# Kernel optimization log

Hardware: AMD Instinct MI355X
Metric: run time of the kernel (lower is better)

The kernel has to match this reference:

```python
import jax, jax.numpy as jnp
from jax import lax
import numpy as np

# NOTE: the original module calls an opaque CUDA 'approximate dot-product' conv kernel.
# Its backward uses EXACT conv2d gradients for input/weight, so the reference forward
# math is the exact conv2d the kernel approximates. `approximate` is a learned scalar
# controlling the hardware approximation level; it does not change the exact-math output.

STRIDE = 1
PAD = (1, 1)  # (padH, padW)


def setup_inputs() -> dict:
    key = jax.random.key(0)
    k1, k2, k3 = jax.random.split(key, 3)
    B, Cin, H, W = 32, 128, 56, 56
    Cout, K = 256, 3
    x = jax.random.normal(k1, (B, Cin, H, W), dtype=jnp.float32)
    # weight init: uniform(-1, 1) per reset_parameters
    weight = jax.random.uniform(k2, (Cout, Cin, K, K), dtype=jnp.float32, minval=-1.0, maxval=1.0)
    fan_in = Cin * K * K
    bound = 1.0 / np.sqrt(fan_in)
    bias = jax.random.uniform(k3, (Cout,), dtype=jnp.float32, minval=-bound, maxval=bound)
    approximate = jnp.ones((1,), dtype=jnp.float32)
    return {"x": x, "weight": weight, "bias": bias, "approximate": approximate}


def reference(x, weight, bias, approximate):
    # Exact conv2d, NCHW input, OIHW kernel. `approximate` controls only the
    # hardware approximation level in the original CUDA kernel.
    out = lax.conv_general_dilated(
        x, weight,
        window_strides=(STRIDE, STRIDE),
        padding=((PAD[0], PAD[0]), (PAD[1], PAD[1])),
        dimension_numbers=("NCHW", "OIHW", "NCHW"),
    )
    return out + bias.reshape(1, -1, 1, 1)
```

## Files before the change

### kernel.cpp

```cpp
#include <hip/hip_runtime.h>


typedef __attribute__((ext_vector_type(8))) short short8;
typedef __attribute__((ext_vector_type(4))) float floatx4;

typedef __attribute__((address_space(1))) const void* gas_ptr;
typedef __attribute__((address_space(3))) void* las_ptr;

__device__ static inline void gl2lds16(const void* g, void* l) {
    __builtin_amdgcn_global_load_lds((gas_ptr)g, (las_ptr)l, 16, 0, 0);
}

__device__ static inline float bf2f(unsigned short u) {
    union { unsigned int i; float f; } x; x.i = ((unsigned int)u) << 16; return x.f;
}
__device__ static inline unsigned short f2bf(float f) {
    union { float f; unsigned int i; } x; x.f = f;
    unsigned int r = (x.i + 0x7FFFu + ((x.i >> 16) & 1u)) >> 16;
    return (unsigned short)r;
}

__device__ static inline bool wave_detect_bf16(const unsigned int* __restrict__ p) {
    const int lane = threadIdx.x & 63;
    int cnt = 0;
#pragma unroll
    for (int r = 0; r < 4; ++r) {
        unsigned int w = p[r * 64 + lane];
        unsigned short lo = (unsigned short)(w & 0xFFFFu);
        int e = (lo >> 7) & 0xFF;
        bool plaus = (lo == 0) || (e >= 96 && e <= 144);
        cnt += (int)__popcll(__ballot(plaus));
    }
    return cnt >= 205;
}

__global__ void wt_repack(const void* __restrict__ wsrc,
                          unsigned short* __restrict__ wt) {
    const bool isbf = wave_detect_bf16((const unsigned int*)wsrc);
    int idx = blockIdx.x * 256 + threadIdx.x;
    int ci  = idx & 127;
    int co  = (idx >> 7) & 255;
    int off = idx >> 15;
    size_t s = (size_t)(co * 128 + ci) * 9 + off;
    float v = isbf ? bf2f(((const unsigned short*)wsrc)[s])
                   : ((const float*)wsrc)[s];
    wt[idx] = f2bf(v);
}

__global__ __launch_bounds__(256) void x_repack(
    const void* __restrict__ xsrc, unsigned short* __restrict__ xp) {
    __shared__ unsigned short tile[56 * 130];
    const int bh  = blockIdx.x;
    const int b   = bh / 58, hp = bh - b * 58;
    const int tid = threadIdx.x;
    unsigned short* row = xp + (size_t)(b * 58 + hp) * 58 * 128;
    if (hp == 0 || hp == 57) {
        uint4 z; z.x = z.y = z.z = z.w = 0u;
        uint4* r = (uint4*)row;
        for (int t = tid; t < 928; t += 256) r[t] = z;
        return;
    }
    const bool isbf = wave_detect_bf16((const unsigned int*)xsrc);
    const int h = hp - 1;
    if (isbf) {
        const unsigned short* xs =
            (const unsigned short*)xsrc + (size_t)b * 128 * 3136 + h * 56;
#pragma unroll
        for (int it = 0; it < 7; ++it) {
            int idx = it * 256 + tid;
            int ci = idx / 14, w4 = idx - ci * 14;
            ushort4 v = *(const ushort4*)(xs + (size_t)ci * 3136 + w4 * 4);
            tile[(w4 * 4 + 0) * 130 + ci] = v.x;
            tile[(w4 * 4 + 1) * 130 + ci] = v.y;
            tile[(w4 * 4 + 2) * 130 + ci] = v.z;
            tile[(w4 * 4 + 3) * 130 + ci] = v.w;
        }
    } else {
        const float* xs = (const float*)xsrc + (size_t)b * 128 * 3136 + h * 56;
#pragma unroll
        for (int it = 0; it < 7; ++it) {
            int idx = it * 256 + tid;
            int ci = idx / 14, w4 = idx - ci * 14;
            float4 v = *(const float4*)(xs + (size_t)ci * 3136 + w4 * 4);
            tile[(w4 * 4 + 0) * 130 + ci] = f2bf(v.x);
            tile[(w4 * 4 + 1) * 130 + ci] = f2bf(v.y);
            tile[(w4 * 4 + 2) * 130 + ci] = f2bf(v.z);
            tile[(w4 * 4 + 3) * 130 + ci] = f2bf(v.w);
        }
    }
    __syncthreads();
#pragma unroll
    for (int it = 0; it < 4; ++it) {
        int k = it * 256 + tid;
        if (k >= 928) break;
        int wq = k >> 4, cc = k & 15;
        uint4 v;
        if (wq == 0 || wq == 57) { v.x = v.y = v.z = v.w = 0u; }
        else {
            const unsigned short* p = &tile[(wq - 1) * 130 + cc * 8];
            union { unsigned short s[8]; uint4 u; } pk;
#pragma unroll
            for (int j = 0; j < 8; ++j) pk.s[j] = p[j];
            v = pk.u;
        }
        *(uint4*)(row + wq * 128 + cc * 8) = v;
    }
}

__global__ __launch_bounds__(256, 2) void conv_mfma(
    const unsigned short* __restrict__ xp,
    const unsigned short* __restrict__ wt,
    const void* __restrict__ bias,
    void* __restrict__ out,
    const void* __restrict__ xorig)
{
    __shared__ __align__(16) char lds[73728];
    const int tid   = threadIdx.x;
    const int lane  = tid & 63;
    const int wv    = tid >> 6;
    const int bid   = blockIdx.x;
    const int ntile = (bid & 7) * 98 + (bid >> 3);

    const bool isbf = wave_detect_bf16((const unsigned int*)xorig);

    const int clg  = (lane & 3) ^ ((lane >> 3) & 3);
    const int rsub = lane >> 2;
    unsigned sbA[4], sbB[2];
    int dbA[4], dbB[2];
#pragma unroll
    for (int s = 0; s < 4; ++s) {
        const int c  = wv * 4 + s;
        const int co = c * 16 + rsub;
        sbA[s] = (unsigned)(co * 256 + clg * 16);
        dbA[s] = c * 1024;
    }
#pragma unroll
    for (int s = 0; s < 2; ++s) {
        const int c = wv * 2 + s;
        const int n = ntile * 128 + c * 16 + rsub;
        const int b = n / 3136, rem = n - b * 3136;
        const int hh = rem / 56, ww = rem - hh * 56;
        sbB[s] = (unsigned)(((b * 58 + hh) * 58 + ww) * 256 + clg * 16);
        dbB[s] = 16384 + c * 1024;
    }

    const int fr = lane & 15;
    const int ph = (lane >> 4) ^ ((fr >> 1) & 3);
    const int wm = wv >> 1;
    const int wn = wv & 1;
    const int aOff = (wm * 128 + fr) * 64 + ph * 16;
    const int bOff = 16384 + (wn * 64 + fr) * 64 + ph * 16;

    floatx4 acc[8][4] = {};

#pragma unroll
    for (int h = 0; h < 2; ++h) {
        char* lb = lds + h * 24576;
        const int q = h & 3;
        const int dA  = q * 64;
        const int dB  = q * 64;
#pragma unroll
        for (int s = 0; s < 4; ++s)
            gl2lds16((const char*)wt + sbA[s] + dA, lb + dbA[s]);
#pragma unroll
        for (int s = 0; s < 2; ++s)
            gl2lds16((const char*)xp + sbB[s] + dB, lb + dbB[s]);
    }
    __builtin_amdgcn_s_waitcnt(0x3F76);
    __builtin_amdgcn_s_barrier();

    int bf_ = 0, st_ = 2;
#pragma unroll 3
    for (int h = 0; h < 36; ++h) {
        const char* la = lds + bf_ * 24576;
        if (h < 34) {
            char* sd = lds + st_ * 24576;
            const int hn  = h + 2;
            const int off = hn >> 2, q = hn & 3;
            const int dA  = off * 65536 + q * 64;
            const int dh_ = off / 3, dw_ = off - dh_ * 3;
            const int dB  = (dh_ * 58 + dw_) * 256 + q * 64;
#pragma unroll
            for (int s = 0; s < 4; ++s)
                gl2lds16((const char*)wt + sbA[s] + dA, sd + dbA[s]);
#pragma unroll
            for (int s = 0; s < 2; ++s)
                gl2lds16((const char*)xp + sbB[s] + dB, sd + dbB[s]);
        }
        short8 af[8], bf[4];
#pragma unroll
        for (int i = 0; i < 8; ++i)
            af[i] = *(const short8*)(la + aOff + i * 1024);
#pragma unroll
        for (int j = 0; j < 4; ++j)
            bf[j] = *(const short8*)(la + bOff + j * 1024);
        __builtin_amdgcn_s_setprio(1);
#pragma unroll
        for (int i = 0; i < 8; ++i)
#pragma unroll
            for (int j = 0; j < 4; ++j)
                acc[i][j] = __builtin_amdgcn_mfma_f32_16x16x32_bf16(
                    af[i], bf[j], acc[i][j], 0, 0, 0);
        __builtin_amdgcn_s_setprio(0);
        if (h < 34) {
            __builtin_amdgcn_s_waitcnt(0x3F76);
            __builtin_amdgcn_s_barrier();
        } else if (h == 34) {
            __builtin_amdgcn_s_waitcnt(0x3F70);
            __builtin_amdgcn_s_barrier();
        }
        bf_ = (bf_ == 2) ? 0 : bf_ + 1;
        st_ = (st_ == 2) ? 0 : st_ + 1;
    }

    const int q4 = (lane >> 4) << 2;
    int nb[4], ns[4];
#pragma unroll
    for (int j = 0; j < 4; ++j) {
        const int n = ntile * 128 + wn * 64 + j * 16 + fr;
        nb[j] = n / 3136;
        ns[j] = n - nb[j] * 3136;
    }
#pragma unroll
    for (int i = 0; i < 8; ++i) {
        const int co = wm * 128 + i * 16 + q4;
        float bv[4];
        if (isbf) {
            const ushort4 bb = *(const ushort4*)((const unsigned short*)bias + co);
            bv[0] = bf2f(bb.x); bv[1] = bf2f(bb.y);
            bv[2] = bf2f(bb.z); bv[3] = bf2f(bb.w);
        } else {
            const float4 bb = *(const float4*)((const float*)bias + co);
            bv[0] = bb.x; bv[1] = bb.y; bv[2] = bb.z; bv[3] = bb.w;
        }
#pragma unroll
        for (int j = 0; j < 4; ++j) {
#pragma unroll
            for (int r = 0; r < 4; ++r) {
                const float v = acc[i][j][r] + bv[r];
                const size_t o = (size_t)nb[j] * 802816 +
                                 (size_t)(co + r) * 3136 + ns[j];
                if (isbf) ((unsigned short*)out)[o] = f2bf(v);
                else      ((float*)out)[o] = v;
            }
        }
    }
}

__global__ void conv_naive(const float* __restrict__ x,
                           const float* __restrict__ w,
                           const float* __restrict__ bias,
                           float* __restrict__ out) {
    long long i = (long long)blockIdx.x * 256 + threadIdx.x;
    if (i >= 25690112LL) return;
    int wo = (int)(i % 56); long long t = i / 56;
    int ho = (int)(t % 56); t /= 56;
    int co = (int)(t % 256); int b = (int)(t / 256);
    float acc = bias[co];
    for (int ci = 0; ci < 128; ++ci)
        for (int dh = 0; dh < 3; ++dh) {
            int hi = ho + dh - 1; if ((unsigned)hi >= 56u) continue;
            for (int dw = 0; dw < 3; ++dw) {
                int wi = wo + dw - 1; if ((unsigned)wi >= 56u) continue;
                acc += x[((size_t)(b * 128 + ci) * 56 + hi) * 56 + wi] *
                       w[((co * 128 + ci) * 3 + dh) * 3 + dw];
            }
        }
    out[i] = acc;
}

extern "C" void kernel_launch(void* const* d_in, const int* in_sizes, int n_in,
                              void* d_out, int out_size, void* d_ws, size_t ws_size,
                              hipStream_t stream) {
    const void* x    = d_in[0];
    const void* w    = d_in[1];
    const void* bias = d_in[2];

    const size_t xp_bytes = (size_t)32 * 58 * 58 * 128 * 2;
    const size_t wt_off   = xp_bytes;
    const size_t wt_bytes = (size_t)9 * 256 * 128 * 2;
    const size_t need     = wt_off + wt_bytes;

    if (ws_size >= need) {
        unsigned short* xp = (unsigned short*)d_ws;
        unsigned short* wt = (unsigned short*)((char*)d_ws + wt_off);
        x_repack<<<32 * 58, 256, 0, stream>>>(x, xp);
        wt_repack<<<1152, 256, 0, stream>>>(w, wt);
        conv_mfma<<<dim3(784, 1, 1), 256, 0, stream>>>(xp, wt, bias, d_out, x);
    } else {
        conv_naive<<<(25690112 + 255) / 256, 256, 0, stream>>>(
            (const float*)x, (const float*)w, (const float*)bias, (float*)d_out);
    }
}
```

Measured before the change: 210.6 us.

## Load weight fragments directly to registers, pre-swizzled, and shrink LDS to input double buffer

The weight repack now writes the weights in MFMA fragment order, so each lane can load its A operands straight from global memory (L2-resident) into registers, double-buffered across iterations. Only the input tile stays in LDS, now a two-stage buffer of 16 KB instead of a three-stage 72 KB buffer. This removes weight traffic through LDS and LDS reads for A, and lowers the shared-memory footprint so more blocks can be resident. In exchange, every wave issues its own global weight loads each iteration, adding latency on the critical path, and the loop keeps 16 extra fragment registers live.

```diff
diff --git a/kernel.cpp b/kernel.cpp
--- a/kernel.cpp
+++ b/kernel.cpp
@@ -37,14 +37,23 @@
 __global__ void wt_repack(const void* __restrict__ wsrc,
                           unsigned short* __restrict__ wt) {
     const bool isbf = wave_detect_bf16((const unsigned int*)wsrc);
-    int idx = blockIdx.x * 256 + threadIdx.x;
-    int ci  = idx & 127;
-    int co  = (idx >> 7) & 255;
-    int off = idx >> 15;
-    size_t s = (size_t)(co * 128 + ci) * 9 + off;
-    float v = isbf ? bf2f(((const unsigned short*)wsrc)[s])
-                   : ((const float*)wsrc)[s];
-    wt[idx] = f2bf(v);
+    int idx  = blockIdx.x * 256 + threadIdx.x;
+    int lane = idx & 63;
+    int i    = (idx >> 6) & 7;
+    int wm   = (idx >> 9) & 1;
+    int q    = (idx >> 10) & 3;
+    int off  = idx >> 12;
+    int co   = wm * 128 + i * 16 + (lane & 15);
+    int ci0  = q * 32 + (lane >> 4) * 8;
+    union { unsigned short s[8]; uint4 u; } pk;
+#pragma unroll
+    for (int e = 0; e < 8; ++e) {
+        size_t s = (size_t)(co * 128 + ci0 + e) * 9 + off;
+        float v = isbf ? bf2f(((const unsigned short*)wsrc)[s])
+                       : ((const float*)wsrc)[s];
+        pk.s[e] = f2bf(v);
+    }
+    *(uint4*)(wt + (size_t)idx * 8) = pk.u;
 }
 
 __global__ __launch_bounds__(256) void x_repack(
@@ -114,7 +123,7 @@
     void* __restrict__ out,
     const void* __restrict__ xorig)
 {
-    __shared__ __align__(16) char lds[73728];
+    __shared__ __align__(16) char lds[16384];
     const int tid   = threadIdx.x;
     const int lane  = tid & 63;
     const int wv    = tid >> 6;
@@ -125,15 +134,7 @@
 
     const int clg  = (lane & 3) ^ ((lane >> 3) & 3);
     const int rsub = lane >> 2;
-    unsigned sbA[4], sbB[2];
-    int dbA[4], dbB[2];
-#pragma unroll
-    for (int s = 0; s < 4; ++s) {
-        const int c  = wv * 4 + s;
-        const int co = c * 16 + rsub;
-        sbA[s] = (unsigned)(co * 256 + clg * 16);
-        dbA[s] = c * 1024;
-    }
+    unsigned sbB[2]; int dbB[2];
 #pragma unroll
     for (int s = 0; s < 2; ++s) {
         const int c = wv * 2 + s;
@@ -141,76 +142,82 @@
         const int b = n / 3136, rem = n - b * 3136;
         const int hh = rem / 56, ww = rem - hh * 56;
         sbB[s] = (unsigned)(((b * 58 + hh) * 58 + ww) * 256 + clg * 16);
-        dbB[s] = 16384 + c * 1024;
+        dbB[s] = c * 1024;
     }
 
     const int fr = lane & 15;
     const int ph = (lane >> 4) ^ ((fr >> 1) & 3);
     const int wm = wv >> 1;
     const int wn = wv & 1;
-    const int aOff = (wm * 128 + fr) * 64 + ph * 16;
-    const int bOff = 16384 + (wn * 64 + fr) * 64 + ph * 16;
+    const int bOff = (wn * 64 + fr) * 64 + ph * 16;
+    const int aSub = wm * 4096 + lane * 8;
 
     floatx4 acc[8][4] = {};
-
-#pragma unroll
-    for (int h = 0; h < 2; ++h) {
-        char* lb = lds + h * 24576;
-        const int q = h & 3;
-        const int dA  = q * 64;
-        const int dB  = q * 64;
-#pragma unroll
-        for (int s = 0; s < 4; ++s)
-            gl2lds16((const char*)wt + sbA[s] + dA, lb + dbA[s]);
-#pragma unroll
-        for (int s = 0; s < 2; ++s)
-            gl2lds16((const char*)xp + sbB[s] + dB, lb + dbB[s]);
-    }
-    __builtin_amdgcn_s_waitcnt(0x3F76);
+    short8 afA[8], afB[8];
+
+#pragma unroll
+    for (int i_ = 0; i_ < 8; ++i_)
+        afA[i_] = *(const short8*)(wt + aSub + i_ * 512);
+    gl2lds16((const char*)xp + sbB[0], lds + dbB[0]);
+    gl2lds16((const char*)xp + sbB[1], lds + dbB[1]);
+    __builtin_amdgcn_s_waitcnt(0x3F70);
     __builtin_amdgcn_s_barrier();
 
-    int bf_ = 0, st_ = 2;
-#pragma unroll 3
-    for (int h = 0; h < 36; ++h) {
-        const char* la = lds + bf_ * 24576;
-        if (h < 34) {
-            char* sd = lds + st_ * 24576;
-            const int hn  = h + 2;
-            const int off = hn >> 2, q = hn & 3;
-            const int dA  = off * 65536 + q * 64;
-            const int dh_ = off / 3, dw_ = off - dh_ * 3;
-            const int dB  = (dh_ * 58 + dw_) * 256 + q * 64;
-#pragma unroll
-            for (int s = 0; s < 4; ++s)
-                gl2lds16((const char*)wt + sbA[s] + dA, sd + dbA[s]);
-#pragma unroll
-            for (int s = 0; s < 2; ++s)
-                gl2lds16((const char*)xp + sbB[s] + dB, sd + dbB[s]);
-        }
-        short8 af[8], bf[4];
-#pragma unroll
-        for (int i = 0; i < 8; ++i)
-            af[i] = *(const short8*)(la + aOff + i * 1024);
-#pragma unroll
-        for (int j = 0; j < 4; ++j)
-            bf[j] = *(const short8*)(la + bOff + j * 1024);
-        __builtin_amdgcn_s_setprio(1);
-#pragma unroll
-        for (int i = 0; i < 8; ++i)
-#pragma unroll
-            for (int j = 0; j < 4; ++j)
-                acc[i][j] = __builtin_amdgcn_mfma_f32_16x16x32_bf16(
-                    af[i], bf[j], acc[i][j], 0, 0, 0);
-        __builtin_amdgcn_s_setprio(0);
-        if (h < 34) {
-            __builtin_amdgcn_s_waitcnt(0x3F76);
-            __builtin_amdgcn_s_barrier();
-        } else if (h == 34) {
-            __builtin_amdgcn_s_waitcnt(0x3F70);
-            __builtin_amdgcn_s_barrier();
-        }
-        bf_ = (bf_ == 2) ? 0 : bf_ + 1;
-        st_ = (st_ == 2) ? 0 : st_ + 1;
+#define BODY(H, AF_USE, AF_LOAD)                                           \
+  {                                                                        \
+    {                                                                      \
+      const unsigned short* aP = wt + (size_t)((H) + 1) * 8192 + aSub;     \
+      _Pragma("unroll")                                                    \
+      for (int i_ = 0; i_ < 8; ++i_)                                       \
+        AF_LOAD[i_] = *(const short8*)(aP + i_ * 512);                     \
+    }                                                                      \
+    {                                                                      \
+      char* sd = lds + (((H) + 1) & 1) * 8192;                             \
+      const int hn = (H) + 1, off_ = hn >> 2, qq = hn & 3;                 \
+      const int dh_ = off_ / 3, dw_ = off_ - dh_ * 3;                      \
+      const int dB = (dh_ * 58 + dw_) * 256 + qq * 64;                     \
+      gl2lds16((const char*)xp + sbB[0] + dB, sd + dbB[0]);                \
+      gl2lds16((const char*)xp + sbB[1] + dB, sd + dbB[1]);                \
+    }                                                                      \
+    short8 bfr[4];                                                         \
+    {                                                                      \
+      const char* la = lds + ((H) & 1) * 8192;                             \
+      bfr[0] = *(const short8*)(la + bOff);                                \
+      bfr[1] = *(const short8*)(la + bOff + 1024);                         \
+      bfr[2] = *(const short8*)(la + bOff + 2048);                         \
+      bfr[3] = *(const short8*)(la + bOff + 3072);                         \
+    }                                                                      \
+    __builtin_amdgcn_s_setprio(1);                                         \
+    _Pragma("unroll")                                                      \
+    for (int i_ = 0; i_ < 8; ++i_) {                                       \
+      _Pragma("unroll")                                                    \
+      for (int j_ = 0; j_ < 4; ++j_)                                       \
+        acc[i_][j_] = __builtin_amdgcn_mfma_f32_16x16x32_bf16(             \
+            AF_USE[i_], bfr[j_], acc[i_][j_], 0, 0, 0);                    \
+    }                                                                      \
+    __builtin_amdgcn_s_setprio(0);                                         \
+    __builtin_amdgcn_s_waitcnt(0x3F70);                                    \
+    __builtin_amdgcn_s_barrier();                                          \
+  }
+
+    for (int h = 0; h < 34; h += 2) {
+        BODY(h,     afA, afB);
+        BODY(h + 1, afB, afA);
+    }
+    BODY(34, afA, afB);
+    {
+        const char* la = lds + 8192;
+        short8 bfr[4];
+        bfr[0] = *(const short8*)(la + bOff);
+        bfr[1] = *(const short8*)(la + bOff + 1024);
+        bfr[2] = *(const short8*)(la + bOff + 2048);
+        bfr[3] = *(const short8*)(la + bOff + 3072);
+#pragma unroll
+        for (int i_ = 0; i_ < 8; ++i_)
+#pragma unroll
+            for (int j_ = 0; j_ < 4; ++j_)
+                acc[i_][j_] = __builtin_amdgcn_mfma_f32_16x16x32_bf16(
+                    afB[i_], bfr[j_], acc[i_][j_], 0, 0, 0);
     }
 
     const int q4 = (lane >> 4) << 2;
@@ -285,7 +292,7 @@
         unsigned short* xp = (unsigned short*)d_ws;
         unsigned short* wt = (unsigned short*)((char*)d_ws + wt_off);
         x_repack<<<32 * 58, 256, 0, stream>>>(x, xp);
-        wt_repack<<<1152, 256, 0, stream>>>(w, wt);
+        wt_repack<<<144, 256, 0, stream>>>(w, wt);
         conv_mfma<<<dim3(784, 1, 1), 256, 0, stream>>>(xp, wt, bias, d_out, x);
     } else {
         conv_naive<<<(25690112 + 255) / 256, 256, 0, stream>>>(
```

Result: no change. 212.1 us (+0.7%).

## Split conv MFMA block across 8 waves with 64x64 per-wave tiles

Applied to the files above, without the earlier changes.

The block grows from 4 to 8 waves. Each wave now computes a 64x64 output sub-tile instead of 128x64, which halves the accumulator registers and the loads per wave. The global-to-LDS staging is redistributed to 3 loads per lane, and the bf16 dtype detection moves after the main loop. The aim is more waves in flight to hide latency. In exchange, LDS fragment reuse per wave drops and barriers now sync 8 waves, while the 72KB LDS still caps occupancy at two blocks per CU.

```diff
diff --git a/kernel.cpp b/kernel.cpp
--- a/kernel.cpp
+++ b/kernel.cpp
@@ -107,7 +107,7 @@
     }
 }
 
-__global__ __launch_bounds__(256, 2) void conv_mfma(
+__global__ __launch_bounds__(512, 4) void conv_mfma(
     const unsigned short* __restrict__ xp,
     const unsigned short* __restrict__ wt,
     const void* __restrict__ bias,
@@ -121,52 +121,43 @@
     const int bid   = blockIdx.x;
     const int ntile = (bid & 7) * 98 + (bid >> 3);
 
-    const bool isbf = wave_detect_bf16((const unsigned int*)xorig);
-
     const int clg  = (lane & 3) ^ ((lane >> 3) & 3);
     const int rsub = lane >> 2;
-    unsigned sbA[4], sbB[2];
-    int dbA[4], dbB[2];
-#pragma unroll
-    for (int s = 0; s < 4; ++s) {
-        const int c  = wv * 4 + s;
+    unsigned sbA[2], sbB;
+    int dbA[2], dbB;
+#pragma unroll
+    for (int s = 0; s < 2; ++s) {
+        const int c  = wv * 2 + s;
         const int co = c * 16 + rsub;
         sbA[s] = (unsigned)(co * 256 + clg * 16);
         dbA[s] = c * 1024;
     }
-#pragma unroll
-    for (int s = 0; s < 2; ++s) {
-        const int c = wv * 2 + s;
-        const int n = ntile * 128 + c * 16 + rsub;
+    {
+        const int n = ntile * 128 + wv * 16 + rsub;
         const int b = n / 3136, rem = n - b * 3136;
         const int hh = rem / 56, ww = rem - hh * 56;
-        sbB[s] = (unsigned)(((b * 58 + hh) * 58 + ww) * 256 + clg * 16);
-        dbB[s] = 16384 + c * 1024;
+        sbB = (unsigned)(((b * 58 + hh) * 58 + ww) * 256 + clg * 16);
+        dbB = 16384 + wv * 1024;
     }
 
     const int fr = lane & 15;
     const int ph = (lane >> 4) ^ ((fr >> 1) & 3);
-    const int wm = wv >> 1;
-    const int wn = wv & 1;
-    const int aOff = (wm * 128 + fr) * 64 + ph * 16;
-    const int bOff = 16384 + (wn * 64 + fr) * 64 + ph * 16;
-
-    floatx4 acc[8][4] = {};
+    const int wm2 = wv >> 1;
+    const int wn2 = wv & 1;
+    const int aOff = (wm2 * 64 + fr) * 64 + ph * 16;
+    const int bOff = 16384 + (wn2 * 64 + fr) * 64 + ph * 16;
+
+    floatx4 acc[4][4] = {};
 
 #pragma unroll
     for (int h = 0; h < 2; ++h) {
         char* lb = lds + h * 24576;
-        const int q = h & 3;
-        const int dA  = q * 64;
-        const int dB  = q * 64;
-#pragma unroll
-        for (int s = 0; s < 4; ++s)
-            gl2lds16((const char*)wt + sbA[s] + dA, lb + dbA[s]);
-#pragma unroll
-        for (int s = 0; s < 2; ++s)
-            gl2lds16((const char*)xp + sbB[s] + dB, lb + dbB[s]);
-    }
-    __builtin_amdgcn_s_waitcnt(0x3F76);
+        const int d = h * 64;
+        gl2lds16((const char*)wt + sbA[0] + d, lb + dbA[0]);
+        gl2lds16((const char*)wt + sbA[1] + d, lb + dbA[1]);
+        gl2lds16((const char*)xp + sbB + d, lb + dbB);
+    }
+    __builtin_amdgcn_s_waitcnt(0x3F73);
     __builtin_amdgcn_s_barrier();
 
     int bf_ = 0, st_ = 2;
@@ -180,30 +171,27 @@
             const int dA  = off * 65536 + q * 64;
             const int dh_ = off / 3, dw_ = off - dh_ * 3;
             const int dB  = (dh_ * 58 + dw_) * 256 + q * 64;
-#pragma unroll
-            for (int s = 0; s < 4; ++s)
-                gl2lds16((const char*)wt + sbA[s] + dA, sd + dbA[s]);
-#pragma unroll
-            for (int s = 0; s < 2; ++s)
-                gl2lds16((const char*)xp + sbB[s] + dB, sd + dbB[s]);
-        }
-        short8 af[8], bf[4];
-#pragma unroll
-        for (int i = 0; i < 8; ++i)
+            gl2lds16((const char*)wt + sbA[0] + dA, sd + dbA[0]);
+            gl2lds16((const char*)wt + sbA[1] + dA, sd + dbA[1]);
+            gl2lds16((const char*)xp + sbB + dB, sd + dbB);
+        }
+        short8 af[4], bf[4];
+#pragma unroll
+        for (int i = 0; i < 4; ++i)
             af[i] = *(const short8*)(la + aOff + i * 1024);
 #pragma unroll
         for (int j = 0; j < 4; ++j)
             bf[j] = *(const short8*)(la + bOff + j * 1024);
         __builtin_amdgcn_s_setprio(1);
 #pragma unroll
-        for (int i = 0; i < 8; ++i)
+        for (int i = 0; i < 4; ++i)
 #pragma unroll
             for (int j = 0; j < 4; ++j)
                 acc[i][j] = __builtin_amdgcn_mfma_f32_16x16x32_bf16(
                     af[i], bf[j], acc[i][j], 0, 0, 0);
         __builtin_amdgcn_s_setprio(0);
         if (h < 34) {
-            __builtin_amdgcn_s_waitcnt(0x3F76);
+            __builtin_amdgcn_s_waitcnt(0x3F73);
             __builtin_amdgcn_s_barrier();
         } else if (h == 34) {
             __builtin_amdgcn_s_waitcnt(0x3F70);
@@ -213,17 +201,19 @@
         st_ = (st_ == 2) ? 0 : st_ + 1;
     }
 
+    const bool isbf = wave_detect_bf16((const unsigned int*)xorig);
+
     const int q4 = (lane >> 4) << 2;
     int nb[4], ns[4];
 #pragma unroll
     for (int j = 0; j < 4; ++j) {
-        const int n = ntile * 128 + wn * 64 + j * 16 + fr;
+        const int n = ntile * 128 + wn2 * 64 + j * 16 + fr;
         nb[j] = n / 3136;
         ns[j] = n - nb[j] * 3136;
     }
 #pragma unroll
-    for (int i = 0; i < 8; ++i) {
-        const int co = wm * 128 + i * 16 + q4;
+    for (int i = 0; i < 4; ++i) {
+        const int co = wm2 * 64 + i * 16 + q4;
         float bv[4];
         if (isbf) {
             const ushort4 bb = *(const ushort4*)((const unsigned short*)bias + co);
@@ -286,7 +276,7 @@
         unsigned short* wt = (unsigned short*)((char*)d_ws + wt_off);
         x_repack<<<32 * 58, 256, 0, stream>>>(x, xp);
         wt_repack<<<1152, 256, 0, stream>>>(w, wt);
-        conv_mfma<<<dim3(784, 1, 1), 256, 0, stream>>>(xp, wt, bias, d_out, x);
+        conv_mfma<<<dim3(784, 1, 1), 512, 0, stream>>>(xp, wt, bias, d_out, x);
     } else {
         conv_naive<<<(25690112 + 255) / 256, 256, 0, stream>>>(
             (const float*)x, (const float*)w, (const float*)bias, (float*)d_out);
```

Result: slower. 232.3 us (+10.3%).
